# Kernel tuning notes

Hardware: AMD Instinct MI355X
Metric: run time of the kernel (lower is better)

## Reference

```python
import jax, jax.numpy as jnp
import numpy as np

HID = 2048; S = 2048; NH = 16
Q_LORA = 1536; KV_LORA = 512
D_NOPE = 128; D_ROPE = 64; D_V = 128
D_QK = D_NOPE + D_ROPE  # 192
EPS = 1e-6


def setup_inputs() -> dict:
    key = jax.random.key(0)
    ks = jax.random.split(key, 8)
    hidden_states = jax.random.normal(ks[0], (1, S, HID), dtype=jnp.float32)
    # real RoPE tables, HF layout: cos/sin = concat(freqs, freqs) along last dim
    inv_freq = 1.0 / (10000.0 ** (np.arange(0, D_ROPE, 2, dtype=np.float32) / D_ROPE))
    t = np.arange(S, dtype=np.float32)
    freqs = np.outer(t, inv_freq)  # [S, D_ROPE//2]
    emb = np.concatenate([freqs, freqs], axis=-1)  # [S, D_ROPE]
    cos = jnp.asarray(np.cos(emb))[None]  # [1, S, D_ROPE]
    sin = jnp.asarray(np.sin(emb))[None]
    def lin(k, fan_in, fan_out):
        return jax.random.normal(k, (fan_in, fan_out), dtype=jnp.float32) / np.sqrt(fan_in)
    return {
        'hidden_states': hidden_states, 'cos': cos, 'sin': sin,
        'w_qa': lin(ks[1], HID, Q_LORA),
        'g_qa': jnp.ones((Q_LORA,), jnp.float32),
        'w_qb': lin(ks[2], Q_LORA, NH * D_QK),
        'w_kva': lin(ks[3], HID, KV_LORA + D_ROPE),
        'g_kva': jnp.ones((KV_LORA,), jnp.float32),
        'w_kvb': lin(ks[4], KV_LORA, NH * (D_NOPE + D_V)),
        'w_o': lin(ks[5], NH * D_V, HID),
    }


def _rmsnorm(x, g):
    var = jnp.mean(x * x, axis=-1, keepdims=True)
    return x * jax.lax.rsqrt(var + EPS) * g


def _deinterleave(x):
    # view (..., d//2, 2) -> transpose -> reshape: even-index dims first, then odd
    b, h, s, d = x.shape
    return x.reshape(b, h, s, d // 2, 2).transpose(0, 1, 2, 4, 3).reshape(b, h, s, d)


def _rotate_half(x):
    x1, x2 = jnp.split(x, 2, axis=-1)
    return jnp.concatenate([-x2, x1], axis=-1)


def _apply_rope(q, k, cos, sin):
    cos = cos[:, None]  # [B,1,S,D]
    sin = sin[:, None]
    q = _deinterleave(q)
    k = _deinterleave(k)
    q_emb = q * cos + _rotate_half(q) * sin
    k_emb = k * cos + _rotate_half(k) * sin
    return q_emb, k_emb


def reference(hidden_states, cos, sin, w_qa, g_qa, w_qb, w_kva, g_kva, w_kvb, w_o):
    bsz, q_len, _ = hidden_states.shape
    # low-rank Q projection
    q = _rmsnorm(hidden_states @ w_qa, g_qa) @ w_qb  # [B,S,NH*D_QK]
    q = q.reshape(bsz, q_len, NH, D_QK).transpose(0, 2, 1, 3)  # [B,NH,S,D_QK]
    q_nope, q_pe = q[..., :D_NOPE], q[..., D_NOPE:]
    # compressed KV + shared rope key
    ckv = hidden_states @ w_kva  # [B,S,KV_LORA+D_ROPE]
    compressed_kv, k_pe = ckv[..., :KV_LORA], ckv[..., KV_LORA:]
    k_pe = k_pe.reshape(bsz, q_len, 1, D_ROPE).transpose(0, 2, 1, 3)  # [B,1,S,D_ROPE]
    kv = (_rmsnorm(compressed_kv, g_kva) @ w_kvb).reshape(bsz, q_len, NH, D_NOPE + D_V).transpose(0, 2, 1, 3)
    k_nope, value_states = kv[..., :D_NOPE], kv[..., D_NOPE:]
    # interleaved RoPE
    q_pe, k_pe = _apply_rope(q_pe, k_pe, cos, sin)
    query_states = jnp.concatenate([q_nope, q_pe], axis=-1)  # [B,NH,S,D_QK]
    key_states = jnp.concatenate([k_nope, jnp.broadcast_to(k_pe, (bsz, NH, q_len, D_ROPE))], axis=-1)
    # causal attention with MLA softmax scale
    scale = D_QK ** (-0.5)
    scores = jnp.einsum('bhqd,bhkd->bhqk', query_states, key_states) * scale
    mask = jnp.tril(jnp.ones((q_len, q_len), dtype=bool))
    scores = jnp.where(mask, scores, jnp.finfo(scores.dtype).min)
    probs = jax.nn.softmax(scores, axis=-1)
    attn = jnp.einsum('bhqk,bhkd->bhqd', probs, value_states)  # [B,NH,S,D_V]
    attn = attn.transpose(0, 2, 1, 3).reshape(bsz, q_len, NH * D_V)
    return attn @ w_o
```

## Files before the change

### kernel.cpp

```cpp
#include <hip/hip_runtime.h>
#include <hip/hip_bf16.h>

#define S_LEN 2048
#define HID_D 2048
#define NHEAD 16
#define QLORA 1536
#define KVLORA 512
#define DNOPE 128
#define DROPE 64
#define DV 128
#define DQK 192
#define NCAT 2176

#define KS_SH (64 * 192)
#define VS_SH (128 * 64)
#define BUF_SH (KS_SH + VS_SH)

typedef __hip_bfloat16 bf16;
typedef __attribute__((ext_vector_type(8))) short short8;
typedef __attribute__((ext_vector_type(4))) short s16x4;
typedef __attribute__((ext_vector_type(4))) float f32x4;

__device__ __forceinline__ float ldE(const float* p) { return *p; }
__device__ __forceinline__ float ldE(const bf16* p) { return __bfloat162float(*p); }
__device__ __forceinline__ void stE(float* p, float v) { *p = v; }
__device__ __forceinline__ void stE(bf16* p, float v) { *p = __float2bfloat16(v); }

__device__ __forceinline__ short bf16bits(float v) {
    __hip_bfloat16 h = __float2bfloat16(v);
    return *reinterpret_cast<short*>(&h);
}

__device__ __forceinline__ float b2f(short s) {
    union { short s; bf16 h; } u;
    u.s = s;
    return __bfloat162float(u.h);
}

__device__ __forceinline__ f32x4 mfma16(short8 a, short8 b, f32x4 c) {
    return __builtin_amdgcn_mfma_f32_16x16x32_bf16(a, b, c, 0, 0, 0);
}

__device__ __forceinline__ void gload16(const void* g, void* l) {
    __builtin_amdgcn_global_load_lds(
        (const __attribute__((address_space(1))) unsigned int*)g,
        (__attribute__((address_space(3))) unsigned int*)l, 16, 0, 0);
}

__global__ void detect_kernel(const void* hidden, int* flag) {
    __shared__ int red[256];
    const int tid = threadIdx.x;
    const bf16* hb = (const bf16*)hidden;
    float a = fabsf(__bfloat162float(hb[tid]));
    red[tid] = (!(a < 64.f) || (a != 0.f && a < 1e-30f)) ? 1 : 0;
    __syncthreads();
    for (int o = 128; o > 0; o >>= 1) {
        if (tid < o) red[tid] += red[tid + o];
        __syncthreads();
    }
    if (tid == 0) *flag = (red[0] > 16) ? 1 : 0;
}

__global__ void convert_kernel(const void* in, bf16* out, int n8, const int* flag) {
    int i = blockIdx.x * 256 + threadIdx.x;
    if (i >= n8) return;
    size_t off = (size_t)i * 8;
    short8 o;
    if (*flag) {
        const float* f = (const float*)in + off;
#pragma unroll
        for (int j = 0; j < 8; ++j) o[j] = bf16bits(f[j]);
    } else {
        o = *(const short8*)((const short*)in + off);
    }
    *(short8*)((short*)out + off) = o;
}

template <int KDIM>
__device__ void transpose_tile(const void* in, bf16* out, int N, int n0, int k0,
                               int roff, int fp32) {
    __shared__ __align__(16) short Ts[64][80];
    const int tid = threadIdx.x;
    const bool inb = n0 < N;
    const int kl = tid >> 4;
    const int nl = (tid & 15) * 4;
#pragma unroll
    for (int p = 0; p < 4; ++p) {
        int k = kl + p * 16;
        float v[4] = {0.f, 0.f, 0.f, 0.f};
        if (inb) {
            if (fp32) {
                const float4 f = *(const float4*)((const float*)in + (size_t)(k0 + k) * N + n0 + nl);
                v[0] = f.x; v[1] = f.y; v[2] = f.z; v[3] = f.w;
            } else {
                const bf16* bp = (const bf16*)in + (size_t)(k0 + k) * N + n0 + nl;
#pragma unroll
                for (int i = 0; i < 4; ++i) v[i] = __bfloat162float(bp[i]);
            }
        }
#pragma unroll
        for (int i = 0; i < 4; ++i) Ts[nl + i][k] = bf16bits(v[i]);
    }
    __syncthreads();
    const int nr = tid >> 2;
    const int kq = (tid & 3) * 16;
    short* op = (short*)out + (size_t)(roff + n0 + nr) * KDIM + k0 + kq;
    *(short8*)op = *(short8*)&Ts[nr][kq];
    *(short8*)(op + 8) = *(short8*)&Ts[nr][kq + 8];
}

__global__ void transpose_kernel(const void* in, bf16* out, int K, int N, int Npad,
                                 const int* flag) {
    __shared__ __align__(16) short Ts[64][80];
    const int tid = threadIdx.x;
    const int n0 = blockIdx.x * 64, k0 = blockIdx.y * 64;
    const bool inb = n0 < N;
    const int fp32 = *flag;
    const int kl = tid >> 4;
    const int nl = (tid & 15) * 4;
#pragma unroll
    for (int p = 0; p < 4; ++p) {
        int k = kl + p * 16;
        float v[4] = {0.f, 0.f, 0.f, 0.f};
        if (inb) {
            if (fp32) {
                const float4 f = *(const float4*)((const float*)in + (size_t)(k0 + k) * N + n0 + nl);
                v[0] = f.x; v[1] = f.y; v[2] = f.z; v[3] = f.w;
            } else {
                const bf16* bp = (const bf16*)in + (size_t)(k0 + k) * N + n0 + nl;
#pragma unroll
                for (int i = 0; i < 4; ++i) v[i] = __bfloat162float(bp[i]);
            }
        }
#pragma unroll
        for (int i = 0; i < 4; ++i) Ts[nl + i][k] = bf16bits(v[i]);
    }
    __syncthreads();
    const int nr = tid >> 2;
    const int kq = (tid & 3) * 16;
    short* op = (short*)out + (size_t)(n0 + nr) * K + k0 + kq;
    *(short8*)op = *(short8*)&Ts[nr][kq];
    *(short8*)(op + 8) = *(short8*)&Ts[nr][kq + 8];
}

__global__ void transpose2_kernel(const void* inA, const void* inB, bf16* out,
                                  const int* flag) {
    const int bx = blockIdx.x;
    const int k0 = blockIdx.y * 64;
    const int fp32 = *flag;
    if (bx < 24) transpose_tile<HID_D>(inA, out, QLORA, bx * 64, k0, 0, fp32);
    else         transpose_tile<HID_D>(inB, out, KVLORA + DROPE, (bx - 24) * 64, k0, QLORA, fp32);
}

template <int MODE, typename TC>
__device__ void mgemm_body(const bf16* __restrict__ A, int lda,
                           const bf16* __restrict__ Bt, int ldb,
                           TC* __restrict__ C, int ldc, int K,
                           bf16* __restrict__ Kn, bf16* __restrict__ Vt) {
    __shared__ __align__(16) short As[128 * 64];
    __shared__ __align__(16) short Bs[128 * 64];
    const int tid = threadIdx.x;
    const int w = tid >> 6, lane = tid & 63;
    const int lg = lane >> 4, ln = lane & 15;
    const int wm = w >> 1, wn = w & 1;
    const int m0 = blockIdx.y * 128, n0 = blockIdx.x * 128;

    const bf16* aP[4];
    const bf16* bP[4];
#pragma unroll
    for (int p = 0; p < 4; ++p) {
        const int cid = tid + p * 256;
        const int row = cid >> 3, cpos = cid & 7;
        const int c = cpos ^ (row & 7);
        aP[p] = A + (size_t)(m0 + row) * lda + c * 8;
        bP[p] = Bt + (size_t)(n0 + row) * ldb + c * 8;
    }
    int aoff[2][4], boff[2][4];
#pragma unroll
    for (int hk = 0; hk < 2; ++hk)
#pragma unroll
        for (int i = 0; i < 4; ++i) {
            const int ra = wm * 64 + i * 16 + ln;
            const int rb = wn * 64 + i * 16 + ln;
            aoff[hk][i] = ra * 64 + ((hk * 4 + lg) ^ (ra & 7)) * 8;
            boff[hk][i] = rb * 64 + ((hk * 4 + lg) ^ (rb & 7)) * 8;
        }

    f32x4 acc[4][4];
#pragma unroll
    for (int i = 0; i < 4; ++i)
#pragma unroll
        for (int j = 0; j < 4; ++j) acc[i][j] = (f32x4){0.f, 0.f, 0.f, 0.f};

    for (int k0 = 0; k0 < K; k0 += 64) {
        __syncthreads();
#pragma unroll
        for (int p = 0; p < 4; ++p) {
            gload16(aP[p] + k0, As + (w + 4 * p) * 512);
            gload16(bP[p] + k0, Bs + (w + 4 * p) * 512);
        }
        __syncthreads();
#pragma unroll
        for (int hk = 0; hk < 2; ++hk) {
            short8 af[4], bfr[4];
#pragma unroll
            for (int i = 0; i < 4; ++i) af[i] = *(const short8*)&As[aoff[hk][i]];
#pragma unroll
            for (int j = 0; j < 4; ++j) bfr[j] = *(const short8*)&Bs[boff[hk][j]];
#pragma unroll
            for (int i = 0; i < 4; ++i)
#pragma unroll
                for (int j = 0; j < 4; ++j) acc[i][j] = mfma16(af[i], bfr[j], acc[i][j]);
        }
    }
    if constexpr (MODE == 2) {
#pragma unroll
        for (int i = 0; i < 4; ++i)
#pragma unroll
            for (int j = 0; j < 4; ++j) {
                const int col = n0 + wn * 64 + j * 16 + ln;
                const int row = m0 + wm * 64 + i * 16 + lg * 4;
                const int h = col >> 8, d = col & 255;
                if (d < DNOPE) {
                    bf16* cp = Kn + (size_t)row * (NHEAD * DNOPE) + h * DNOPE + d;
#pragma unroll
                    for (int r = 0; r < 4; ++r)
                        cp[(size_t)r * (NHEAD * DNOPE)] = __float2bfloat16(acc[i][j][r]);
                } else {
                    s16x4 pk;
#pragma unroll
                    for (int r = 0; r < 4; ++r) pk[r] = bf16bits(acc[i][j][r]);
                    *(s16x4*)(Vt + (size_t)(h * DV + (d - DNOPE)) * S_LEN + row) = pk;
                }
            }
    } else {
#pragma unroll
        for (int i = 0; i < 4; ++i)
#pragma unroll
            for (int j = 0; j < 4; ++j) {
                TC* cp = C + (size_t)(m0 + wm * 64 + i * 16 + lg * 4) * ldc + n0 + wn * 64 +
                         j * 16 + ln;
#pragma unroll
                for (int r = 0; r < 4; ++r)
                    stE(cp + (size_t)r * ldc, acc[i][j][r]);
            }
    }
}

template <int MODE>
__global__ __launch_bounds__(256, 2)
void mgemm_kernel(const bf16* A, int lda, const bf16* Bt, int ldb, void* C, int ldc,
                  int K, const int* flag, bf16* Kn, bf16* Vt) {
    if (MODE == 1 && *flag)
        mgemm_body<1, float>(A, lda, Bt, ldb, (float*)C, ldc, K, nullptr, nullptr);
    else if (MODE == 2)
        mgemm_body<2, bf16>(A, lda, Bt, ldb, (bf16*)C, ldc, K, Kn, Vt);
    else
        mgemm_body<0, bf16>(A, lda, Bt, ldb, (bf16*)C, ldc, K, nullptr, nullptr);
}

template <typename TG>
__device__ void rmsnorm_row(const bf16* __restrict__ xr, const TG* __restrict__ g,
                            bf16* __restrict__ yr, int len) {
    const int tid = threadIdx.x;
    float ss = 0.f;
    for (int i = tid; i < len; i += 256) {
        float v = __bfloat162float(xr[i]);
        ss += v * v;
    }
    __shared__ float red[256];
    red[tid] = ss;
    __syncthreads();
    for (int o = 128; o > 0; o >>= 1) {
        if (tid < o) red[tid] += red[tid + o];
        __syncthreads();
    }
    const float scale = rsqrtf(red[0] / (float)len + 1e-6f);
    for (int i = tid; i < len; i += 256)
        yr[i] = __float2bfloat16(__bfloat162float(xr[i]) * scale * ldE(&g[i]));
}

__global__ void rmsnorm2_kernel(bf16* qk, const void* g_qa, const void* g_kva,
                                bf16* ckvn, const int* flag) {
    const int bid = blockIdx.x;
    if (*flag) {
        if (bid < S_LEN)
            rmsnorm_row<float>(qk + (size_t)bid * NCAT, (const float*)g_qa,
                               qk + (size_t)bid * NCAT, QLORA);
        else {
            const int s = bid - S_LEN;
            rmsnorm_row<float>(qk + (size_t)s * NCAT + QLORA, (const float*)g_kva,
                               ckvn + (size_t)s * KVLORA, KVLORA);
        }
    } else {
        if (bid < S_LEN)
            rmsnorm_row<bf16>(qk + (size_t)bid * NCAT, (const bf16*)g_qa,
                              qk + (size_t)bid * NCAT, QLORA);
        else {
            const int s = bid - S_LEN;
            rmsnorm_row<bf16>(qk + (size_t)s * NCAT + QLORA, (const bf16*)g_kva,
                              ckvn + (size_t)s * KVLORA, KVLORA);
        }
    }
}

template <typename TG>
__device__ void rope_body(bf16* __restrict__ q, const bf16* __restrict__ ckv,
                          bf16* __restrict__ kpe, const TG* __restrict__ cosb,
                          const TG* __restrict__ sinb) {
    const int s = blockIdx.x;
    const int tid = threadIdx.x;
    float x0 = 0.f, x1 = 0.f, c = 0.f, sn = 0.f;
    bf16* qbase = nullptr;
    int p = 0;
    const bool isq = tid < 512;
    const bool active = tid < 544;
    if (active) {
        if (isq) {
            const int h = tid >> 5;
            p = tid & 31;
            qbase = q + (size_t)s * (NHEAD * DQK) + h * DQK + DNOPE;
            x0 = __bfloat162float(qbase[2 * p]);
            x1 = __bfloat162float(qbase[2 * p + 1]);
        } else {
            p = tid - 512;
            const bf16* kb = ckv + (size_t)s * NCAT + KVLORA;
            x0 = __bfloat162float(kb[2 * p]);
            x1 = __bfloat162float(kb[2 * p + 1]);
        }
        c = ldE(&cosb[s * 64 + p]);
        sn = ldE(&sinb[s * 64 + p]);
    }
    __syncthreads();
    if (active) {
        if (isq) {
            qbase[p] = __float2bfloat16(x0 * c - x1 * sn);
            qbase[p + 32] = __float2bfloat16(x1 * c + x0 * sn);
        } else {
            kpe[s * 64 + p] = __float2bfloat16(x0 * c - x1 * sn);
            kpe[s * 64 + p + 32] = __float2bfloat16(x1 * c + x0 * sn);
        }
    }
}

__global__ void rope_kernel(bf16* q, const bf16* ckv, bf16* kpe,
                            const void* cosb, const void* sinb, const int* flag) {
    if (*flag) rope_body<float>(q, ckv, kpe, (const float*)cosb, (const float*)sinb);
    else       rope_body<bf16>(q, ckv, kpe, (const bf16*)cosb, (const bf16*)sinb);
}

__global__ __launch_bounds__(256, 2)
void fattn_kernel(const bf16* __restrict__ q, const bf16* __restrict__ kn,
                  const bf16* __restrict__ vt, const bf16* __restrict__ kpe,
                  bf16* __restrict__ attn, bf16* __restrict__ Opart, float* __restrict__ ml) {
    const int nf = blockIdx.x;
    const int xcd = nf & 7;
    const int j = nf >> 3;
    const int bx = j & 31;
    const int h = (j >> 5) * 8 + xcd;
    int qt, part, nparts;
    if (bx < 15)      { qt = 15 - bx / 3;        part = bx % 3;        nparts = 3; }
    else if (bx < 27) { qt = 10 - (bx - 15) / 2; part = (bx - 15) & 1; nparts = 2; }
    else              { qt = 31 - bx;            part = 0;             nparts = 1; }
    const int nt = 2 * qt + 2;
    const int bsz = nt / nparts, rr = nt % nparts;
    const int t0 = part * bsz + (part < rr ? part : rr);
    const int t1 = t0 + bsz + (part < rr ? 1 : 0);
    const int q0 = qt * 128;

    const int tid = threadIdx.x;
    const int w = tid >> 6;
    const int l = tid & 63;
    const int lg = l >> 4;
    const int ln = l & 15;

    __shared__ __align__(16) short KV[2][BUF_SH];

    int offK[6], sK[6];
    bool isn[6];
#pragma unroll
    for (int p = 0; p < 6; ++p) {
        const int cid = tid + p * 256;
        const int row = cid / 24;
        const int cpos = cid % 24;
        const int c = (cpos & 24) | ((cpos & 7) ^ (row & 7));
        if (c < 16) {
            offK[p] = row * (NHEAD * DNOPE) + h * DNOPE + c * 8;
            sK[p] = NHEAD * DNOPE;
            isn[p] = true;
        } else {
            offK[p] = row * DROPE + (c - 16) * 8;
            sK[p] = DROPE;
            isn[p] = false;
        }
    }
    int offV[4];
#pragma unroll
    for (int p = 0; p < 4; ++p) {
        const int cid = tid + p * 256;
        const int row = cid >> 3;
        const int cc = (cid & 7) ^ (row & 7);
        offV[p] = (h * DV + row) * S_LEN + cc * 8;
    }

    short8 qf[2][6];
#pragma unroll
    for (int i = 0; i < 2; ++i) {
        const short* qrow =
            (const short*)(q + (size_t)(q0 + i * 64 + w * 16 + ln) * (NHEAD * DQK) + h * DQK);
#pragma unroll
        for (int ks = 0; ks < 6; ++ks)
            qf[i][ks] = *(const short8*)(qrow + ks * 32 + lg * 8);
    }

    f32x4 O[2][8];
#pragma unroll
    for (int i = 0; i < 2; ++i)
#pragma unroll
        for (int ct = 0; ct < 8; ++ct) O[i][ct] = (f32x4){0.f, 0.f, 0.f, 0.f};
    float m_[2][4], l_[2][4];
#pragma unroll
    for (int i = 0; i < 2; ++i)
#pragma unroll
        for (int r = 0; r < 4; ++r) { m_[i][r] = -1e30f; l_[i][r] = 0.f; }
    const float scale = 0.07216878364870322f;

    {
        const int k0 = t0 * 64;
#pragma unroll
        for (int p = 0; p < 6; ++p) {
            const bf16* sp = (isn[p] ? kn : kpe) + (size_t)offK[p] + (size_t)k0 * sK[p];
            gload16(sp, &KV[0][0] + (w + 4 * p) * 512);
        }
#pragma unroll
        for (int p = 0; p < 4; ++p)
            gload16(vt + (size_t)offV[p] + k0, &KV[0][KS_SH] + (w + 4 * p) * 512);
    }

    for (int t = t0; t < t1; ++t) {
        const int cur = (t - t0) & 1;
        short* Ks = &KV[cur][0];
        short* Vs = &KV[cur][KS_SH];
        if (t + 1 < t1) {
            const int k0n = (t + 1) * 64;
            short* KsN = &KV[cur ^ 1][0];
            short* VsN = &KV[cur ^ 1][KS_SH];
#pragma unroll
            for (int p = 0; p < 6; ++p) {
                const bf16* sp = (isn[p] ? kn : kpe) + (size_t)offK[p] + (size_t)k0n * sK[p];
                gload16(sp, KsN + (w + 4 * p) * 512);
            }
#pragma unroll
            for (int p = 0; p < 4; ++p)
                gload16(vt + (size_t)offV[p] + k0n, VsN + (w + 4 * p) * 512);
            asm volatile("s_waitcnt vmcnt(10)" ::: "memory");
        } else {
            asm volatile("s_waitcnt vmcnt(0)" ::: "memory");
        }
        __builtin_amdgcn_s_barrier();

        const int k0 = t * 64;
        f32x4 S[2][4];
#pragma unroll
        for (int i = 0; i < 2; ++i)
#pragma unroll
            for (int c = 0; c < 4; ++c) S[i][c] = (f32x4){0.f, 0.f, 0.f, 0.f};
        __builtin_amdgcn_s_setprio(1);
#pragma unroll
        for (int ks = 0; ks < 6; ++ks) {
            const int kch = ks * 4 + lg;
#pragma unroll
            for (int c = 0; c < 4; ++c) {
                short8 kf = *(const short8*)&Ks[(size_t)(c * 16 + ln) * 192 +
                                               (size_t)(kch ^ (ln & 7)) * 8];
                S[0][c] = mfma16(qf[0][ks], kf, S[0][c]);
                S[1][c] = mfma16(qf[1][ks], kf, S[1][c]);
            }
        }
        __builtin_amdgcn_s_setprio(0);

        const int d0 = k0 - q0;
#pragma unroll
        for (int i = 0; i < 2; ++i)
#pragma unroll
            for (int c = 0; c < 4; ++c)
#pragma unroll
                for (int r = 0; r < 4; ++r) {
                    float v = S[i][c][r] * scale;
                    if (d0 > -64 &&
                        (d0 + c * 16 + ln) > (i * 64 + w * 16 + lg * 4 + r)) v = -1e30f;
                    S[i][c][r] = v;
                }

        float alpha[2][4];
#pragma unroll
        for (int i = 0; i < 2; ++i)
#pragma unroll
            for (int r = 0; r < 4; ++r) {
                float mx = fmaxf(fmaxf(S[i][0][r], S[i][1][r]), fmaxf(S[i][2][r], S[i][3][r]));
#pragma unroll
                for (int d = 1; d < 16; d <<= 1) mx = fmaxf(mx, __shfl_xor(mx, d));
                float mn = fmaxf(m_[i][r], mx);
                alpha[i][r] = __expf(m_[i][r] - mn);
                m_[i][r] = mn;
                float rs = 0.f;
#pragma unroll
                for (int c = 0; c < 4; ++c) {
                    float p = __expf(S[i][c][r] - mn);
                    S[i][c][r] = p;
                    rs += p;
                }
#pragma unroll
                for (int d = 1; d < 16; d <<= 1) rs += __shfl_xor(rs, d);
                l_[i][r] = l_[i][r] * alpha[i][r] + rs;
            }
#pragma unroll
        for (int i = 0; i < 2; ++i)
#pragma unroll
            for (int ct = 0; ct < 8; ++ct)
#pragma unroll
                for (int r = 0; r < 4; ++r) O[i][ct][r] *= alpha[i][r];

        __builtin_amdgcn_s_barrier();
        short* Pb = Ks;
#pragma unroll
        for (int i = 0; i < 2; ++i)
#pragma unroll
            for (int c = 0; c < 4; ++c)
#pragma unroll
                for (int r = 0; r < 4; ++r)
                    Pb[(size_t)(i * 64 + w * 16 + lg * 4 + r) * 70 + c * 16 + ln] =
                        bf16bits(S[i][c][r]);

        __builtin_amdgcn_s_setprio(1);
#pragma unroll
        for (int ks = 0; ks < 2; ++ks) {
            short8 pf0 = *(const short8*)&Pb[(size_t)(w * 16 + ln) * 70 + ks * 32 + lg * 8];
            short8 pf1 = *(const short8*)&Pb[(size_t)(64 + w * 16 + ln) * 70 + ks * 32 + lg * 8];
#pragma unroll
            for (int ct = 0; ct < 8; ++ct) {
                short8 vf = *(const short8*)&Vs[(size_t)(ct * 16 + ln) * 64 +
                                               (size_t)((ks * 4 + lg) ^ (ln & 7)) * 8];
                O[0][ct] = mfma16(pf0, vf, O[0][ct]);
                O[1][ct] = mfma16(pf1, vf, O[1][ct]);
            }
        }
        __builtin_amdgcn_s_setprio(0);
        __builtin_amdgcn_s_barrier();
    }

    if (nparts == 1) {
#pragma unroll
        for (int i = 0; i < 2; ++i)
#pragma unroll
            for (int r = 0; r < 4; ++r) {
                float inv = 1.f / l_[i][r];
                bf16* orow = attn + (size_t)(q0 + i * 64 + w * 16 + lg * 4 + r) * (NHEAD * DV) +
                             h * DV;
#pragma unroll
                for (int ct = 0; ct < 8; ++ct)
                    orow[ct * 16 + ln] = __float2bfloat16(O[i][ct][r] * inv);
            }
    } else {
        const int mlslot = h * 27 + (qt <= 10 ? (qt - 5) * 2 + part : 12 + (qt - 11) * 3 + part);
        float* mlp = ml + (size_t)mlslot * 128 * 2;
        if (part == 0) {
#pragma unroll
            for (int i = 0; i < 2; ++i)
#pragma unroll
                for (int r = 0; r < 4; ++r) {
                    const int rowb = i * 64 + w * 16 + lg * 4 + r;
                    bf16* orow = attn + (size_t)(q0 + rowb) * (NHEAD * DV) + h * DV;
#pragma unroll
                    for (int ct = 0; ct < 8; ++ct)
                        orow[ct * 16 + ln] = __float2bfloat16(O[i][ct][r]);
                    if (ln == 0) {
                        mlp[rowb * 2] = m_[i][r];
                        mlp[rowb * 2 + 1] = l_[i][r];
                    }
                }
        } else {
            const int oslot = h * 16 + (qt <= 10 ? (qt - 5) : 6 + (qt - 11) * 2 + (part - 1));
            bf16* op = Opart + (size_t)oslot * 128 * DV;
#pragma unroll
            for (int i = 0; i < 2; ++i)
#pragma unroll
                for (int r = 0; r < 4; ++r) {
                    const int rowb = i * 64 + w * 16 + lg * 4 + r;
#pragma unroll
                    for (int ct = 0; ct < 8; ++ct)
                        op[(size_t)rowb * DV + ct * 16 + ln] = __float2bfloat16(O[i][ct][r]);
                    if (ln == 0) {
                        mlp[rowb * 2] = m_[i][r];
                        mlp[rowb * 2 + 1] = l_[i][r];
                    }
                }
        }
    }
}

__global__ void reduce_kernel(const bf16* __restrict__ Opart, const float* __restrict__ ml,
                              bf16* __restrict__ attn) {
    const int qq = blockIdx.x;
    const int h = blockIdx.y;
    const int qt = 5 + qq;
    const int np = (qt <= 10) ? 2 : 3;
    const int q0 = qt * 128;
    const int tid = threadIdx.x;
    const int row = tid >> 1;
    const int dh = (tid & 1) * 64;
    float mp[3], lp[3], f[3];
    float mm = -1e30f;
    for (int p = 0; p < np; ++p) {
        const int msl = h * 27 + (qt <= 10 ? (qt - 5) * 2 + p : 12 + (qt - 11) * 3 + p);
        mp[p] = ml[((size_t)msl * 128 + row) * 2];
        lp[p] = ml[((size_t)msl * 128 + row) * 2 + 1];
        mm = fmaxf(mm, mp[p]);
    }
    float denom = 0.f;
    for (int p = 0; p < np; ++p) {
        f[p] = __expf(mp[p] - mm);
        denom += f[p] * lp[p];
    }
    const float inv = 1.f / denom;
    const int os1 = h * 16 + (qt <= 10 ? (qt - 5) : 6 + (qt - 11) * 2);
    bf16* arow = attn + (size_t)(q0 + row) * (NHEAD * DV) + h * DV + dh;
    const bf16* o1 = Opart + ((size_t)os1 * 128 + row) * DV + dh;
    const bf16* o2 = o1 + (size_t)128 * DV;
#pragma unroll
    for (int jc = 0; jc < 8; ++jc) {
        short8 a = *(const short8*)(arow + jc * 8);
        short8 b1 = *(const short8*)(o1 + jc * 8);
        short8 b2 = (np == 3) ? *(const short8*)(o2 + jc * 8) : b1;
        short8 o;
#pragma unroll
        for (int e = 0; e < 8; ++e) {
            float v = f[0] * b2f(a[e]) + f[1] * b2f(b1[e]);
            if (np == 3) v += f[2] * b2f(b2[e]);
            o[e] = bf16bits(v * inv);
        }
        *(short8*)(arow + jc * 8) = o;
    }
}

extern "C" void kernel_launch(void* const* d_in, const int* in_sizes, int n_in,
                              void* d_out, int out_size, void* d_ws, size_t ws_size,
                              hipStream_t stream) {
    const void* hidden = d_in[0];
    const void* cosb   = d_in[1];
    const void* sinb   = d_in[2];
    const void* w_qa   = d_in[3];
    const void* g_qa   = d_in[4];
    const void* w_qb   = d_in[5];
    const void* w_kva  = d_in[6];
    const void* g_kva  = d_in[7];
    const void* w_kvb  = d_in[8];
    const void* w_o    = d_in[9];

    bf16* ws = (bf16*)d_ws;
    bf16* qk   = ws;
    bf16* ckvn = qk + (size_t)S_LEN * NCAT;
    bf16* q    = ckvn + (size_t)S_LEN * KVLORA;
    bf16* kn   = q + (size_t)S_LEN * NHEAD * DQK;
    bf16* vtb  = kn + (size_t)S_LEN * NHEAD * DNOPE;
    bf16* kpe  = vtb + (size_t)NHEAD * DV * S_LEN;
    bf16* hbf  = kpe + (size_t)S_LEN * DROPE;
    int* flag  = (int*)(hbf + (size_t)S_LEN * HID_D);
    bf16* attn = ws;
    float* ml  = (float*)(ws + (size_t)S_LEN * HID_D);
    bf16* Opart = hbf;
    bf16* BtCat = kn;
    bf16* wqbT  = kn;
    bf16* wkvbT = hbf;
    bf16* W4    = q;

    detect_kernel<<<1, 256, 0, stream>>>(hidden, flag);
    convert_kernel<<<(S_LEN * HID_D / 8 + 255) / 256, 256, 0, stream>>>(
        hidden, hbf, S_LEN * HID_D / 8, flag);

    transpose2_kernel<<<dim3(34, HID_D / 64), 256, 0, stream>>>(w_qa, w_kva, BtCat, flag);
    mgemm_kernel<0><<<dim3(NCAT / 128, S_LEN / 128), 256, 0, stream>>>(
        hbf, HID_D, BtCat, HID_D, qk, NCAT, HID_D, flag, nullptr, nullptr);
    rmsnorm2_kernel<<<2 * S_LEN, 256, 0, stream>>>(qk, g_qa, g_kva, ckvn, flag);
    transpose_kernel<<<dim3(NHEAD * DQK / 64, QLORA / 64), 256, 0, stream>>>(
        w_qb, wqbT, QLORA, NHEAD * DQK, NHEAD * DQK, flag);
    mgemm_kernel<0><<<dim3(NHEAD * DQK / 128, S_LEN / 128), 256, 0, stream>>>(
        qk, NCAT, wqbT, QLORA, q, NHEAD * DQK, QLORA, flag, nullptr, nullptr);
    transpose_kernel<<<dim3(NHEAD * (DNOPE + DV) / 64, KVLORA / 64), 256, 0, stream>>>(
        w_kvb, wkvbT, KVLORA, NHEAD * (DNOPE + DV), NHEAD * (DNOPE + DV), flag);
    mgemm_kernel<2><<<dim3(NHEAD * (DNOPE + DV) / 128, S_LEN / 128), 256, 0, stream>>>(
        ckvn, KVLORA, wkvbT, KVLORA, kn, NHEAD * (DNOPE + DV), KVLORA, flag, kn, vtb);
    rope_kernel<<<S_LEN, 576, 0, stream>>>(q, qk + QLORA, kpe, cosb, sinb, flag);
    fattn_kernel<<<dim3(512), 256, 0, stream>>>(q, kn, vtb, kpe, attn, Opart, ml);
    reduce_kernel<<<dim3(11, NHEAD), 256, 0, stream>>>(Opart, ml, attn);
    transpose_kernel<<<dim3(HID_D / 64, HID_D / 64), 256, 0, stream>>>(
        w_o, W4, HID_D, HID_D, HID_D, flag);
    mgemm_kernel<1><<<dim3(HID_D / 128, S_LEN / 128), 256, 0, stream>>>(
        attn, NHEAD * DV, W4, HID_D, d_out, HID_D, HID_D, flag, nullptr, nullptr);
}
```

Before: 346.6 us.

## Add XCD-aware block swizzle to GEMMs, raise occupancy, and merge weight transposes

```diff
diff --git a/kernel.cpp b/kernel.cpp
--- a/kernel.cpp
+++ b/kernel.cpp
@@ -150,6 +150,20 @@
     const int fp32 = *flag;
     if (bx < 24) transpose_tile<HID_D>(inA, out, QLORA, bx * 64, k0, 0, fp32);
     else         transpose_tile<HID_D>(inB, out, KVLORA + DROPE, (bx - 24) * 64, k0, QLORA, fp32);
+}
+
+__global__ void transposeQK_kernel(const void* inQ, bf16* outQ,
+                                   const void* inKV, bf16* outKV, const int* flag) {
+    const int bid = blockIdx.x;
+    const int fp32 = *flag;
+    if (bid < 1152) {
+        const int n0 = (bid % 48) * 64, k0 = (bid / 48) * 64;
+        transpose_tile<QLORA>(inQ, outQ, NHEAD * DQK, n0, k0, 0, fp32);
+    } else {
+        const int b = bid - 1152;
+        const int n0 = (b % 64) * 64, k0 = (b / 64) * 64;
+        transpose_tile<KVLORA>(inKV, outKV, NHEAD * (DNOPE + DV), n0, k0, 0, fp32);
+    }
 }
 
 template <int MODE, typename TC>
@@ -163,17 +177,21 @@
     const int w = tid >> 6, lane = tid & 63;
     const int lg = lane >> 4, ln = lane & 15;
     const int wm = w >> 1, wn = w & 1;
-    const int m0 = blockIdx.y * 128, n0 = blockIdx.x * 128;
-
-    const bf16* aP[4];
-    const bf16* bP[4];
+
+    const int nbx = gridDim.x;
+    const int flat = blockIdx.y * nbx + blockIdx.x;
+    const int cpx = (nbx * gridDim.y) >> 3;
+    const int swz = (flat & 7) * cpx + (flat >> 3);
+    const int m0 = (swz / nbx) * 128, n0 = (swz % nbx) * 128;
+
+    int aO[4], bO[4];
 #pragma unroll
     for (int p = 0; p < 4; ++p) {
         const int cid = tid + p * 256;
         const int row = cid >> 3, cpos = cid & 7;
         const int c = cpos ^ (row & 7);
-        aP[p] = A + (size_t)(m0 + row) * lda + c * 8;
-        bP[p] = Bt + (size_t)(n0 + row) * ldb + c * 8;
+        aO[p] = (m0 + row) * lda + c * 8;
+        bO[p] = (n0 + row) * ldb + c * 8;
     }
     int aoff[2][4], boff[2][4];
 #pragma unroll
@@ -196,8 +214,8 @@
         __syncthreads();
 #pragma unroll
         for (int p = 0; p < 4; ++p) {
-            gload16(aP[p] + k0, As + (w + 4 * p) * 512);
-            gload16(bP[p] + k0, Bs + (w + 4 * p) * 512);
+            gload16(A + (size_t)aO[p] + k0, As + (w + 4 * p) * 512);
+            gload16(Bt + (size_t)bO[p] + k0, Bs + (w + 4 * p) * 512);
         }
         __syncthreads();
 #pragma unroll
@@ -248,7 +266,7 @@
 }
 
 template <int MODE>
-__global__ __launch_bounds__(256, 2)
+__global__ __launch_bounds__(256, 3)
 void mgemm_kernel(const bf16* A, int lda, const bf16* Bt, int ldb, void* C, int ldc,
                   int K, const int* flag, bf16* Kn, bf16* Vt) {
     if (MODE == 1 && *flag)
@@ -682,12 +700,9 @@
     mgemm_kernel<0><<<dim3(NCAT / 128, S_LEN / 128), 256, 0, stream>>>(
         hbf, HID_D, BtCat, HID_D, qk, NCAT, HID_D, flag, nullptr, nullptr);
     rmsnorm2_kernel<<<2 * S_LEN, 256, 0, stream>>>(qk, g_qa, g_kva, ckvn, flag);
-    transpose_kernel<<<dim3(NHEAD * DQK / 64, QLORA / 64), 256, 0, stream>>>(
-        w_qb, wqbT, QLORA, NHEAD * DQK, NHEAD * DQK, flag);
+    transposeQK_kernel<<<dim3(1664), 256, 0, stream>>>(w_qb, wqbT, w_kvb, wkvbT, flag);
     mgemm_kernel<0><<<dim3(NHEAD * DQK / 128, S_LEN / 128), 256, 0, stream>>>(
         qk, NCAT, wqbT, QLORA, q, NHEAD * DQK, QLORA, flag, nullptr, nullptr);
-    transpose_kernel<<<dim3(NHEAD * (DNOPE + DV) / 64, KVLORA / 64), 256, 0, stream>>>(
-        w_kvb, wkvbT, KVLORA, NHEAD * (DNOPE + DV), NHEAD * (DNOPE + DV), flag);
     mgemm_kernel<2><<<dim3(NHEAD * (DNOPE + DV) / 128, S_LEN / 128), 256, 0, stream>>>(
         ckvn, KVLORA, wkvbT, KVLORA, kn, NHEAD * (DNOPE + DV), KVLORA, flag, kn, vtb);
     rope_kernel<<<S_LEN, 576, 0, stream>>>(q, qk + QLORA, kpe, cosb, sinb, flag);
```

After: 349.5 us. About the same (+0.8%).
